# Optimization experiments

Hardware: AMD Instinct MI355X
Metric: run time of the kernel (lower is better)

The kernel has to match this reference:

```python
import jax, jax.numpy as jnp
import numpy as np

N_SAMPLES = 50
BETA = 1.0
EPSILON = 1e-6

def setup_inputs() -> dict:
    key = jax.random.key(0)
    k1, k2, k3, k4 = jax.random.split(key, 4)
    B, D = 8192, 64
    mean = jax.random.normal(k1, (B, D), dtype=jnp.float32)
    variance = jax.random.uniform(k2, (B, D), dtype=jnp.float32)
    noise = jax.random.normal(k3, (N_SAMPLES, B, D), dtype=jnp.float32)
    target = jax.random.normal(k4, (B, D), dtype=jnp.float32)
    return {"mean": mean, "variance": variance, "noise": noise, "target": target}

def reference(mean, variance, noise, target):
    n = noise.shape[0]
    std = jnp.sqrt(variance + EPSILON)                      # [B, D]
    samples = mean[None] + noise * std[None]                # [n, B, D]
    # E[||X - y||] (elementwise abs, mean over samples)
    first_term = jnp.abs(samples - target[None]).mean(axis=0)  # [B, D]
    # sum_{i<j} |s_i - s_j| via sort identity: for sorted x, equals sum_k (2k - n + 1) x_k
    s_sorted = jnp.sort(samples, axis=0)                    # [n, B, D]
    coef = (2.0 * jnp.arange(n, dtype=s_sorted.dtype) - (n - 1))  # [n]
    pair_sum = jnp.einsum('s,sbd->bd', coef, s_sorted)      # [B, D]
    n_pairs = n * (n - 1) / 2.0
    second_term = pair_sum / n_pairs
    energy_score = first_term - (BETA / 2.0) * second_term  # [B, D]
    return energy_score.mean()                               # reduction='mean'
```

## Files before the change

kernel.cpp:

```cpp
#include <hip/hip_runtime.h>
#include <float.h>

#define NS 50
#define NP 64
#define B_DIM 8192
#define D_DIM 64
#define BD (B_DIM * D_DIM)
#define BLOCK 256
#define EPT 2
#define GRID2 (BD / (BLOCK * EPT))

__device__ __forceinline__ float block_reduce(float e, int tid) {
    #pragma unroll
    for (int off = 32; off > 0; off >>= 1)
        e += __shfl_down(e, off, 64);
    __shared__ float wsum[BLOCK / 64];
    const int lane = tid & 63;
    const int wid  = tid >> 6;
    if (lane == 0) wsum[wid] = e;
    __syncthreads();
    float bs = 0.0f;
    if (tid == 0) {
        #pragma unroll
        for (int w = 0; w < BLOCK / 64; ++w) bs += wsum[w];
    }
    return bs;
}

__device__ __forceinline__ float elem_energy(float* s, float m, float sd, float t) {
    float f0 = 0.0f, f1 = 0.0f;
    #pragma unroll
    for (int k = 0; k < NS; ++k) {
        s[k] = fmaf(s[k], sd, m);
        float d = fabsf(s[k] - t);
        if (k & 1) f1 += d;
        else       f0 += d;
    }
    #pragma unroll
    for (int k = NS; k < NP; ++k) s[k] = FLT_MAX;

    #pragma unroll
    for (int k = 2; k <= NP; k <<= 1) {
        #pragma unroll
        for (int j = k >> 1; j > 0; j >>= 1) {
            #pragma unroll
            for (int i = 0; i < NP; ++i) {
                const int l = i ^ j;
                if (l > i) {
                    const bool up = ((i & k) == 0);
                    float x = s[i], y = s[l];
                    float lo = fminf(x, y);
                    float hi = fmaxf(x, y);
                    s[i] = up ? lo : hi;
                    s[l] = up ? hi : lo;
                }
            }
        }
    }

    float p0 = 0.0f, p1 = 0.0f;
    #pragma unroll
    for (int k = 0; k < NS; ++k) {
        const float c = (float)(2 * k - (NS - 1));
        if (k & 1) p1 = fmaf(c, s[k], p1);
        else       p0 = fmaf(c, s[k], p0);
    }
    return (f0 + f1) * (1.0f / NS) - (p0 + p1) * (1.0f / 2450.0f);
}

__device__ __forceinline__ float energy_pair(const float* __restrict__ mean,
                                             const float* __restrict__ variance,
                                             const float* __restrict__ noise,
                                             const float* __restrict__ target,
                                             float* park, int tid, int col0) {
    float2 f2[NS];
    const unsigned voff = (unsigned)col0 * 4u;
    #pragma unroll
    for (int k = 0; k < NS; ++k) {
        const unsigned off_k = voff + (unsigned)k * (unsigned)(BD * 4);
        asm volatile("global_load_dwordx2 %0, %1, %2"
                     : "=v"(f2[k])
                     : "v"(off_k), "s"(noise));
    }

    const float2 mv = *(const float2*)(mean + col0);
    const float2 vv = *(const float2*)(variance + col0);
    const float2 tv = *(const float2*)(target + col0);

    asm volatile("s_waitcnt vmcnt(0)" ::: "memory");
    __builtin_amdgcn_sched_barrier(0);

    #pragma unroll
    for (int k = 0; k < NS; ++k) park[k * BLOCK + tid] = f2[k].y;

    float s[NP];
    #pragma unroll
    for (int k = 0; k < NS; ++k) s[k] = f2[k].x;
    float e = elem_energy(s, mv.x, sqrtf(vv.x + 1e-6f), tv.x);

    #pragma unroll
    for (int k = 0; k < NS; ++k) s[k] = park[k * BLOCK + tid];
    e += elem_energy(s, mv.y, sqrtf(vv.y + 1e-6f), tv.y);

    return e * (1.0f / (float)BD);
}

__global__ __launch_bounds__(BLOCK, 3) void energy_partial_kernel(
    const float* __restrict__ mean, const float* __restrict__ variance,
    const float* __restrict__ noise, const float* __restrict__ target,
    float* __restrict__ partial) {
    __shared__ float park[NS * BLOCK];
    const int tid  = threadIdx.x;
    const int wg   = (blockIdx.x & 7) * (GRID2 / 8) + (blockIdx.x >> 3);
    const int col0 = wg * (BLOCK * EPT) + tid * EPT;
    float e = energy_pair(mean, variance, noise, target, park, tid, col0);
    float bs = block_reduce(e, tid);
    if (tid == 0) partial[blockIdx.x] = bs;
}

__global__ __launch_bounds__(BLOCK) void reduce_partial_kernel(
    const float* __restrict__ partial, float* __restrict__ out) {
    float e = 0.0f;
    #pragma unroll
    for (int i = 0; i < GRID2 / BLOCK; ++i)
        e += partial[i * BLOCK + threadIdx.x];
    float bs = block_reduce(e, threadIdx.x);
    if (threadIdx.x == 0) out[0] = bs;
}

__global__ __launch_bounds__(BLOCK, 3) void energy_atomic_kernel(
    const float* __restrict__ mean, const float* __restrict__ variance,
    const float* __restrict__ noise, const float* __restrict__ target,
    float* __restrict__ out) {
    __shared__ float park[NS * BLOCK];
    const int tid  = threadIdx.x;
    const int wg   = (blockIdx.x & 7) * (GRID2 / 8) + (blockIdx.x >> 3);
    const int col0 = wg * (BLOCK * EPT) + tid * EPT;
    float e = energy_pair(mean, variance, noise, target, park, tid, col0);
    float bs = block_reduce(e, tid);
    if (tid == 0) atomicAdd(out, bs);
}

extern "C" void kernel_launch(void* const* d_in, const int* in_sizes, int n_in,
                              void* d_out, int out_size, void* d_ws, size_t ws_size,
                              hipStream_t stream) {
    const float* mean     = (const float*)d_in[0];
    const float* variance = (const float*)d_in[1];
    const float* noise    = (const float*)d_in[2];
    const float* target   = (const float*)d_in[3];
    float* out = (float*)d_out;

    if (ws_size >= (size_t)GRID2 * sizeof(float)) {
        float* partial = (float*)d_ws;
        energy_partial_kernel<<<GRID2, BLOCK, 0, stream>>>(mean, variance, noise,
                                                           target, partial);
        reduce_partial_kernel<<<1, BLOCK, 0, stream>>>(partial, out);
    } else {
        hipMemsetAsync(out, 0, sizeof(float), stream);
        energy_atomic_kernel<<<GRID2, BLOCK, 0, stream>>>(mean, variance, noise,
                                                          target, out);
    }
}
```

Before: 33.23 us.

## Split noise loads per element and overlap second column's loads with first sort

Each thread now handles two columns a block-width apart instead of two adjacent columns. It issues 50 dword loads for each column into separate register arrays. It waits only for the first 50 loads (vmcnt(50)) before sorting column A, so column B's loads stay in flight while that sort runs. The LDS parking buffer is removed. The cost is more register pressure from holding two 64-float arrays plus the in-flight loads, which may cause spills or lower occupancy under launch_bounds(256,3). Dword loads also replace dwordx2 loads, but coalescing is preserved because adjacent threads now read adjacent columns.

```diff
diff --git a/kernel.cpp b/kernel.cpp
--- a/kernel.cpp
+++ b/kernel.cpp
@@ -8,7 +8,7 @@
 #define BD (B_DIM * D_DIM)
 #define BLOCK 256
 #define EPT 2
-#define GRID2 (BD / (BLOCK * EPT))
+#define GRIDN (BD / (BLOCK * EPT))
 
 __device__ __forceinline__ float block_reduce(float e, int tid) {
     #pragma unroll
@@ -68,39 +68,42 @@
     return (f0 + f1) * (1.0f / NS) - (p0 + p1) * (1.0f / 2450.0f);
 }
 
-__device__ __forceinline__ float energy_pair(const float* __restrict__ mean,
-                                             const float* __restrict__ variance,
-                                             const float* __restrict__ noise,
-                                             const float* __restrict__ target,
-                                             float* park, int tid, int col0) {
-    float2 f2[NS];
-    const unsigned voff = (unsigned)col0 * 4u;
+__device__ __forceinline__ float energy_pipelined(
+    const float* __restrict__ mean, const float* __restrict__ variance,
+    const float* __restrict__ noise, const float* __restrict__ target,
+    int colA, int colB) {
+
+    float mA = mean[colA],     mB = mean[colB];
+    float vA = variance[colA], vB = variance[colB];
+    float tA = target[colA],   tB = target[colB];
+    float sdA = sqrtf(vA + 1e-6f);
+    float sdB = sqrtf(vB + 1e-6f);
+    asm volatile("" : "+v"(mA), "+v"(tA), "+v"(mB), "+v"(tB), "+v"(sdA), "+v"(sdB));
+
+    float a[NP], b[NP];
+    const unsigned offA = (unsigned)colA * 4u;
+    const unsigned offB = (unsigned)colB * 4u;
     #pragma unroll
     for (int k = 0; k < NS; ++k) {
-        const unsigned off_k = voff + (unsigned)k * (unsigned)(BD * 4);
-        asm volatile("global_load_dwordx2 %0, %1, %2"
-                     : "=v"(f2[k])
-                     : "v"(off_k), "s"(noise));
+        const unsigned ok = offA + (unsigned)k * (unsigned)(BD * 4);
+        asm volatile("global_load_dword %0, %1, %2"
+                     : "=v"(a[k]) : "v"(ok), "s"(noise));
+    }
+    #pragma unroll
+    for (int k = 0; k < NS; ++k) {
+        const unsigned ok = offB + (unsigned)k * (unsigned)(BD * 4);
+        asm volatile("global_load_dword %0, %1, %2"
+                     : "=v"(b[k]) : "v"(ok), "s"(noise));
     }
 
-    const float2 mv = *(const float2*)(mean + col0);
-    const float2 vv = *(const float2*)(variance + col0);
-    const float2 tv = *(const float2*)(target + col0);
+    asm volatile("s_waitcnt vmcnt(50)" ::: "memory");
+    __builtin_amdgcn_sched_barrier(0);
+    float e = elem_energy(a, mA, sdA, tA);
+    __builtin_amdgcn_sched_barrier(0);
 
     asm volatile("s_waitcnt vmcnt(0)" ::: "memory");
     __builtin_amdgcn_sched_barrier(0);
-
-    #pragma unroll
-    for (int k = 0; k < NS; ++k) park[k * BLOCK + tid] = f2[k].y;
-
-    float s[NP];
-    #pragma unroll
-    for (int k = 0; k < NS; ++k) s[k] = f2[k].x;
-    float e = elem_energy(s, mv.x, sqrtf(vv.x + 1e-6f), tv.x);
-
-    #pragma unroll
-    for (int k = 0; k < NS; ++k) s[k] = park[k * BLOCK + tid];
-    e += elem_energy(s, mv.y, sqrtf(vv.y + 1e-6f), tv.y);
+    e += elem_energy(b, mB, sdB, tB);
 
     return e * (1.0f / (float)BD);
 }
@@ -109,11 +112,12 @@
     const float* __restrict__ mean, const float* __restrict__ variance,
     const float* __restrict__ noise, const float* __restrict__ target,
     float* __restrict__ partial) {
-    __shared__ float park[NS * BLOCK];
     const int tid  = threadIdx.x;
-    const int wg   = (blockIdx.x & 7) * (GRID2 / 8) + (blockIdx.x >> 3);
-    const int col0 = wg * (BLOCK * EPT) + tid * EPT;
-    float e = energy_pair(mean, variance, noise, target, park, tid, col0);
+    const int wg   = (blockIdx.x & 7) * (GRIDN / 8) + (blockIdx.x >> 3);
+    const int base = wg * (BLOCK * EPT);
+    const int colA = base + tid;
+    const int colB = base + BLOCK + tid;
+    float e = energy_pipelined(mean, variance, noise, target, colA, colB);
     float bs = block_reduce(e, tid);
     if (tid == 0) partial[blockIdx.x] = bs;
 }
@@ -122,7 +126,7 @@
     const float* __restrict__ partial, float* __restrict__ out) {
     float e = 0.0f;
     #pragma unroll
-    for (int i = 0; i < GRID2 / BLOCK; ++i)
+    for (int i = 0; i < GRIDN / BLOCK; ++i)
         e += partial[i * BLOCK + threadIdx.x];
     float bs = block_reduce(e, threadIdx.x);
     if (threadIdx.x == 0) out[0] = bs;
@@ -132,11 +136,11 @@
     const float* __restrict__ mean, const float* __restrict__ variance,
     const float* __restrict__ noise, const float* __restrict__ target,
     float* __restrict__ out) {
-    __shared__ float park[NS * BLOCK];
     const int tid  = threadIdx.x;
-    const int wg   = (blockIdx.x & 7) * (GRID2 / 8) + (blockIdx.x >> 3);
-    const int col0 = wg * (BLOCK * EPT) + tid * EPT;
-    float e = energy_pair(mean, variance, noise, target, park, tid, col0);
+    const int wg   = (blockIdx.x & 7) * (GRIDN / 8) + (blockIdx.x >> 3);
+    const int base = wg * (BLOCK * EPT);
+    float e = energy_pipelined(mean, variance, noise, target,
+                               base + tid, base + BLOCK + tid);
     float bs = block_reduce(e, tid);
     if (tid == 0) atomicAdd(out, bs);
 }
@@ -150,14 +154,14 @@
     const float* target   = (const float*)d_in[3];
     float* out = (float*)d_out;
 
-    if (ws_size >= (size_t)GRID2 * sizeof(float)) {
+    if (ws_size >= (size_t)GRIDN * sizeof(float)) {
         float* partial = (float*)d_ws;
-        energy_partial_kernel<<<GRID2, BLOCK, 0, stream>>>(mean, variance, noise,
+        energy_partial_kernel<<<GRIDN, BLOCK, 0, stream>>>(mean, variance, noise,
                                                            target, partial);
         reduce_partial_kernel<<<1, BLOCK, 0, stream>>>(partial, out);
     } else {
         hipMemsetAsync(out, 0, sizeof(float), stream);
-        energy_atomic_kernel<<<GRID2, BLOCK, 0, stream>>>(mean, variance, noise,
+        energy_atomic_kernel<<<GRIDN, BLOCK, 0, stream>>>(mean, variance, noise,
                                                           target, out);
     }
 }
```

After: 34.12 us. 1.03x slower.

## Sort two columns together as packed fp16 pairs in bitonic network

Applied to the files above, without the earlier changes.

Converts each thread's two columns of samples into packed half-precision pairs and runs a single bitonic sort with packed min/max. This replaces two separate fp32 sorts and drops the LDS parking buffer. It aims to halve sorting ALU work and register pressure, and relaxes the launch bounds occupancy hint. The risk is reduced accuracy, since sorted values used in the pairwise term are rounded to fp16.

```diff
diff --git a/kernel.cpp b/kernel.cpp
--- a/kernel.cpp
+++ b/kernel.cpp
@@ -8,7 +8,9 @@
 #define BD (B_DIM * D_DIM)
 #define BLOCK 256
 #define EPT 2
-#define GRID2 (BD / (BLOCK * EPT))
+#define GRIDN (BD / (BLOCK * EPT))
+
+typedef __fp16 f16x2 __attribute__((ext_vector_type(2)));
 
 __device__ __forceinline__ float block_reduce(float e, int tid) {
     #pragma unroll
@@ -27,17 +29,46 @@
     return bs;
 }
 
-__device__ __forceinline__ float elem_energy(float* s, float m, float sd, float t) {
-    float f0 = 0.0f, f1 = 0.0f;
+__device__ __forceinline__ float energy_pair_packed(
+    const float* __restrict__ mean, const float* __restrict__ variance,
+    const float* __restrict__ noise, const float* __restrict__ target,
+    int col0) {
+
+    const float2 mv = *(const float2*)(mean + col0);
+    const float2 vv = *(const float2*)(variance + col0);
+    const float2 tv = *(const float2*)(target + col0);
+    float mA = mv.x, mB = mv.y;
+    float tA = tv.x, tB = tv.y;
+    float sdA = sqrtf(vv.x + 1e-6f);
+    float sdB = sqrtf(vv.y + 1e-6f);
+    asm volatile("" : "+v"(mA), "+v"(tA), "+v"(sdA), "+v"(mB), "+v"(tB), "+v"(sdB));
+
+    float2 f2[NS];
+    const unsigned voff = (unsigned)col0 * 4u;
     #pragma unroll
     for (int k = 0; k < NS; ++k) {
-        s[k] = fmaf(s[k], sd, m);
-        float d = fabsf(s[k] - t);
-        if (k & 1) f1 += d;
-        else       f0 += d;
+        const unsigned ok = voff + (unsigned)k * (unsigned)(BD * 4);
+        asm volatile("global_load_dwordx2 %0, %1, %2"
+                     : "=v"(f2[k]) : "v"(ok), "s"(noise));
     }
+    asm volatile("s_waitcnt vmcnt(0)" ::: "memory");
+    __builtin_amdgcn_sched_barrier(0);
+
+    float fA0 = 0.0f, fA1 = 0.0f, fB0 = 0.0f, fB1 = 0.0f;
+    f16x2 p[NP];
     #pragma unroll
-    for (int k = NS; k < NP; ++k) s[k] = FLT_MAX;
+    for (int k = 0; k < NS; ++k) {
+        float sa = fmaf(f2[k].x, sdA, mA);
+        float sb = fmaf(f2[k].y, sdB, mB);
+        float dA = fabsf(sa - tA);
+        float dB = fabsf(sb - tB);
+        if (k & 1) { fA1 += dA; fB1 += dB; }
+        else       { fA0 += dA; fB0 += dB; }
+        p[k] = __builtin_amdgcn_cvt_pkrtz(sa, sb);
+    }
+    const f16x2 pad = {(__fp16)65504.0f, (__fp16)65504.0f};
+    #pragma unroll
+    for (int k = NS; k < NP; ++k) p[k] = pad;
 
     #pragma unroll
     for (int k = 2; k <= NP; k <<= 1) {
@@ -48,72 +79,39 @@
                 const int l = i ^ j;
                 if (l > i) {
                     const bool up = ((i & k) == 0);
-                    float x = s[i], y = s[l];
-                    float lo = fminf(x, y);
-                    float hi = fmaxf(x, y);
-                    s[i] = up ? lo : hi;
-                    s[l] = up ? hi : lo;
+                    f16x2 x = p[i], y = p[l];
+                    f16x2 lo = __builtin_elementwise_min(x, y);
+                    f16x2 hi = __builtin_elementwise_max(x, y);
+                    p[i] = up ? lo : hi;
+                    p[l] = up ? hi : lo;
                 }
             }
         }
     }
 
-    float p0 = 0.0f, p1 = 0.0f;
+    float pA0 = 0.0f, pA1 = 0.0f, pB0 = 0.0f, pB1 = 0.0f;
     #pragma unroll
     for (int k = 0; k < NS; ++k) {
         const float c = (float)(2 * k - (NS - 1));
-        if (k & 1) p1 = fmaf(c, s[k], p1);
-        else       p0 = fmaf(c, s[k], p0);
-    }
-    return (f0 + f1) * (1.0f / NS) - (p0 + p1) * (1.0f / 2450.0f);
-}
-
-__device__ __forceinline__ float energy_pair(const float* __restrict__ mean,
-                                             const float* __restrict__ variance,
-                                             const float* __restrict__ noise,
-                                             const float* __restrict__ target,
-                                             float* park, int tid, int col0) {
-    float2 f2[NS];
-    const unsigned voff = (unsigned)col0 * 4u;
-    #pragma unroll
-    for (int k = 0; k < NS; ++k) {
-        const unsigned off_k = voff + (unsigned)k * (unsigned)(BD * 4);
-        asm volatile("global_load_dwordx2 %0, %1, %2"
-                     : "=v"(f2[k])
-                     : "v"(off_k), "s"(noise));
+        float sa = (float)p[k][0];
+        float sb = (float)p[k][1];
+        if (k & 1) { pA1 = fmaf(c, sa, pA1); pB1 = fmaf(c, sb, pB1); }
+        else       { pA0 = fmaf(c, sa, pA0); pB0 = fmaf(c, sb, pB0); }
     }
 
-    const float2 mv = *(const float2*)(mean + col0);
-    const float2 vv = *(const float2*)(variance + col0);
-    const float2 tv = *(const float2*)(target + col0);
-
-    asm volatile("s_waitcnt vmcnt(0)" ::: "memory");
-    __builtin_amdgcn_sched_barrier(0);
-
-    #pragma unroll
-    for (int k = 0; k < NS; ++k) park[k * BLOCK + tid] = f2[k].y;
-
-    float s[NP];
-    #pragma unroll
-    for (int k = 0; k < NS; ++k) s[k] = f2[k].x;
-    float e = elem_energy(s, mv.x, sqrtf(vv.x + 1e-6f), tv.x);
-
-    #pragma unroll
-    for (int k = 0; k < NS; ++k) s[k] = park[k * BLOCK + tid];
-    e += elem_energy(s, mv.y, sqrtf(vv.y + 1e-6f), tv.y);
-
+    float e = (fA0 + fA1 + fB0 + fB1) * (1.0f / NS)
+            - (pA0 + pA1 + pB0 + pB1) * (1.0f / 2450.0f);
     return e * (1.0f / (float)BD);
 }
 
-__global__ __launch_bounds__(BLOCK, 3) void energy_partial_kernel(
+__global__ __launch_bounds__(BLOCK, 2) void energy_partial_kernel(
     const float* __restrict__ mean, const float* __restrict__ variance,
     const float* __restrict__ noise, const float* __restrict__ target,
     float* __restrict__ partial) {
-    __shared__ float park[NS * BLOCK];
     const int tid  = threadIdx.x;
-    const int wg   = (blockIdx.x & 7) * (GRID2 / 8) + (blockIdx.x >> 3);
+    const int wg   = (blockIdx.x & 7) * (GRIDN / 8) + (blockIdx.x >> 3);
     const int col0 = wg * (BLOCK * EPT) + tid * EPT;
-    float e = energy_pair(mean, variance, noise, target, park, tid, col0);
+    float e = energy_pair_packed(mean, variance, noise, target, col0);
     float bs = block_reduce(e, tid);
     if (tid == 0) partial[blockIdx.x] = bs;
 }
@@ -122,21 +120,20 @@
     const float* __restrict__ partial, float* __restrict__ out) {
     float e = 0.0f;
     #pragma unroll
-    for (int i = 0; i < GRID2 / BLOCK; ++i)
+    for (int i = 0; i < GRIDN / BLOCK; ++i)
         e += partial[i * BLOCK + threadIdx.x];
     float bs = block_reduce(e, threadIdx.x);
     if (threadIdx.x == 0) out[0] = bs;
 }
 
-__global__ __launch_bounds__(BLOCK, 3) void energy_atomic_kernel(
+__global__ __launch_bounds__(BLOCK, 2) void energy_atomic_kernel(
     const float* __restrict__ mean, const float* __restrict__ variance,
     const float* __restrict__ noise, const float* __restrict__ target,
     float* __restrict__ out) {
-    __shared__ float park[NS * BLOCK];
     const int tid  = threadIdx.x;
-    const int wg   = (blockIdx.x & 7) * (GRID2 / 8) + (blockIdx.x >> 3);
+    const int wg   = (blockIdx.x & 7) * (GRIDN / 8) + (blockIdx.x >> 3);
     const int col0 = wg * (BLOCK * EPT) + tid * EPT;
-    float e = energy_pair(mean, variance, noise, target, park, tid, col0);
+    float e = energy_pair_packed(mean, variance, noise, target, col0);
     float bs = block_reduce(e, tid);
     if (tid == 0) atomicAdd(out, bs);
 }
@@ -150,14 +147,14 @@
     const float* target   = (const float*)d_in[3];
     float* out = (float*)d_out;
 
-    if (ws_size >= (size_t)GRID2 * sizeof(float)) {
+    if (ws_size >= (size_t)GRIDN * sizeof(float)) {
         float* partial = (float*)d_ws;
-        energy_partial_kernel<<<GRID2, BLOCK, 0, stream>>>(mean, variance, noise,
+        energy_partial_kernel<<<GRIDN, BLOCK, 0, stream>>>(mean, variance, noise,
                                                            target, partial);
         reduce_partial_kernel<<<1, BLOCK, 0, stream>>>(partial, out);
     } else {
-        hipMemsetAsync(out, 0, sizeof(float), stream);
-        energy_atomic_kernel<<<GRID2, BLOCK, 0, stream>>>(mean, variance, noise,
+        (void)hipMemsetAsync(out, 0, sizeof(float), stream);
+        energy_atomic_kernel<<<GRIDN, BLOCK, 0, stream>>>(mean, variance, noise,
                                                           target, out);
     }
 }
```

New measurement: 28.45 us. 14.4% less time.
